# Kernel tuning notes

Measured on AMD Instinct MI355X. Metric: run time of the kernel, lower is better.

## Reference

```python
import jax, jax.numpy as jnp
import numpy as np

N, F_IN, H, F_OUT, E = 50000, 128, 8, 16, 800000


def setup_inputs() -> dict:
    key = jax.random.key(0)
    ks = jax.random.split(key, 10)
    x = jax.random.normal(ks[0], (N, F_IN), dtype=jnp.float32)
    edge_index = jax.random.randint(ks[1], (2, E), 0, N, dtype=jnp.int64 if jax.config.read('jax_enable_x64') else jnp.int32)
    edge_prob = jax.random.uniform(ks[2], (E, 1), dtype=jnp.float32)
    s = 1.0 / np.sqrt(F_IN)
    Wp = jax.random.normal(ks[3], (H * F_OUT, F_IN), dtype=jnp.float32) * s
    Wt = jax.random.normal(ks[4], (H * F_OUT, 1), dtype=jnp.float32)
    a_src = jax.random.normal(ks[5], (H, F_OUT), dtype=jnp.float32) * 0.1
    a_trg = jax.random.normal(ks[6], (H, F_OUT), dtype=jnp.float32) * 0.1
    a_tp = jax.random.normal(ks[7], (H, F_OUT), dtype=jnp.float32) * 0.1
    Wskip = jax.random.normal(ks[8], (H * F_OUT, F_IN), dtype=jnp.float32) * s
    bias = jnp.zeros((H * F_OUT,), dtype=jnp.float32)
    return {"x": x, "edge_index": edge_index, "edge_prob": edge_prob,
            "Wp": Wp, "Wt": Wt, "a_src": a_src, "a_trg": a_trg,
            "a_tp": a_tp, "Wskip": Wskip, "bias": bias}


def reference(x, edge_index, edge_prob, Wp, Wt, a_src, a_trg, a_tp, Wskip, bias):
    n = x.shape[0]
    h, f = a_src.shape
    src, trg = edge_index[0], edge_index[1]
    # node projection: [N, H, F_out]
    proj = (x @ Wp.T).reshape(n, h, f)
    # transition-prob projection: [E, H, F_out]
    trans = (edge_prob @ Wt.T).reshape(-1, h, f)
    # per-node source/target scores [N, H], per-edge prob score [E, H]
    s_src = jnp.einsum('nhf,hf->nh', proj, a_src)
    s_trg = jnp.einsum('nhf,hf->nh', proj, a_trg)
    s_tp = jnp.einsum('ehf,hf->eh', trans, a_tp)
    scores = jax.nn.leaky_relu(s_src[src] + s_trg[trg] + s_tp, negative_slope=0.2)
    # global-max-shifted exp, segment softmax over target nodes
    e = jnp.exp(scores - jnp.max(scores))
    denom = jax.ops.segment_sum(e, trg, num_segments=n)
    attn = e / (denom[trg] + 1e-16)  # [E, H]
    weighted = proj[src] * attn[..., None]  # [E, H, F_out]
    out = jax.ops.segment_sum(weighted, trg, num_segments=n)  # [N, H, F_out]
    # skip connection (F_out != F_in -> skip_proj path), concat heads, bias, ELU
    out = out + (x @ Wskip.T).reshape(n, h, f)
    out = out.reshape(n, h * f) + bias
    return jax.nn.elu(out)
```

## Files before the change

### kernel.cpp

```cpp
#include <hip/hip_runtime.h>
#include <hip/hip_fp16.h>
#include <math.h>

constexpr int Nn  = 50000;
constexpr int FIN = 128;
constexpr int NH  = 8;
constexpr int FO  = 16;
constexpr int HF  = 128;
constexpr int NWR = 272;
constexpr int NPREP = NWR / 2;
constexpr int NBLK64 = (Nn + 63) / 64;
constexpr int NSCAN = (Nn + 255) / 256;

typedef _Float16 f16x8 __attribute__((ext_vector_type(8)));
typedef float    f32x4 __attribute__((ext_vector_type(4)));

__global__ __launch_bounds__(256) void k_pc(
    const float* __restrict__ Wp, const float* __restrict__ Wskip,
    const float* __restrict__ a_src, const float* __restrict__ a_trg,
    const float* __restrict__ Wt, const float* __restrict__ a_tp,
    _Float16* __restrict__ Wh, float* __restrict__ ctp,
    const int* __restrict__ trg, int* __restrict__ deg,
    int* __restrict__ rank, int E)
{
    const int bid = blockIdx.x;
    if (bid < NPREP) {
        if (bid == 0 && threadIdx.x < NH) {
            int h = threadIdx.x;
            float s = 0.f;
            #pragma unroll
            for (int f = 0; f < FO; ++f) s += Wt[h * FO + f] * a_tp[h * FO + f];
            ctp[h] = s;
        }
        const int o = bid * 2 + (threadIdx.x >> 7);
        const int k = threadIdx.x & 127;
        float v;
        if (o < 128)      v = Wp[o * FIN + k];
        else if (o < 256) v = Wskip[(o - 128) * FIN + k];
        else if (o < 264) {
            const int h = o - 256;
            float s = 0.f;
            #pragma unroll
            for (int f = 0; f < FO; ++f)
                s += a_src[h * FO + f] * Wp[(h * FO + f) * FIN + k];
            v = s;
        } else {
            const int h = o - 264;
            float s = 0.f;
            #pragma unroll
            for (int f = 0; f < FO; ++f)
                s += a_trg[h * FO + f] * Wp[(h * FO + f) * FIN + k];
            v = s;
        }
        Wh[o * FIN + k] = (_Float16)v;
        return;
    }

    int e = (bid - NPREP) * 256 + threadIdx.x;
    if (e < E) rank[e] = atomicAdd(&deg[trg[e]], 1);
}

__global__ __launch_bounds__(256) void k_scan1(const int* __restrict__ deg,
                                               int* __restrict__ partial)
{
    __shared__ int lds[256];
    int t = threadIdx.x, i = blockIdx.x * 256 + t;
    lds[t] = (i < Nn) ? deg[i] : 0;
    __syncthreads();
    for (int off = 128; off > 0; off >>= 1) {
        if (t < off) lds[t] += lds[t + off];
        __syncthreads();
    }
    if (t == 0) partial[blockIdx.x] = lds[0];
}

__global__ __launch_bounds__(256) void k_scan3(const int* __restrict__ deg,
                                               const int* __restrict__ partial,
                                               int* __restrict__ pos)
{
    __shared__ int lds[256], lds2[256];
    const int t = threadIdx.x;
    const int i = blockIdx.x * 256 + t;
    lds2[t] = (t < NSCAN) ? partial[t] : 0;
    __syncthreads();
    for (int off = 1; off < 256; off <<= 1) {
        int u = (t >= off) ? lds2[t - off] : 0;
        __syncthreads();
        lds2[t] += u;
        __syncthreads();
    }
    const int base = (blockIdx.x == 0) ? 0 : lds2[blockIdx.x - 1];
    int v = (i < Nn) ? deg[i] : 0;
    lds[t] = v;
    __syncthreads();
    for (int off = 1; off < 256; off <<= 1) {
        int u = (t >= off) ? lds[t - off] : 0;
        __syncthreads();
        lds[t] += u;
        __syncthreads();
    }
    if (i < Nn) pos[i] = base + lds[t] - v;
}

__global__ __launch_bounds__(256) void k_fn(
    const int* __restrict__ src, const int* __restrict__ trg,
    const float* __restrict__ prob, const int* __restrict__ rank,
    const int* __restrict__ pos, unsigned int* __restrict__ spk,
    const float* __restrict__ x, const _Float16* __restrict__ Wh,
    const float* __restrict__ bias,
    __half* __restrict__ projA, float* __restrict__ out,
    float* __restrict__ s_pair, int E, int nbFill)
{
    const int bid = blockIdx.x;

    if (bid < nbFill) {
        int e4 = bid * 256 + threadIdx.x;
        if (e4 * 4 < E) {
            int4   s4 = reinterpret_cast<const int4*>(src)[e4];
            int4   t4 = reinterpret_cast<const int4*>(trg)[e4];
            float4 p4 = reinterpret_cast<const float4*>(prob)[e4];
            int4   r4 = reinterpret_cast<const int4*>(rank)[e4];
            int    sv[4] = {s4.x, s4.y, s4.z, s4.w};
            int    tv[4] = {t4.x, t4.y, t4.z, t4.w};
            int    rv[4] = {r4.x, r4.y, r4.z, r4.w};
            float  pv[4] = {p4.x, p4.y, p4.z, p4.w};
            #pragma unroll
            for (int i = 0; i < 4; ++i) {
                int slot = pos[tv[i]] + rv[i];
                spk[slot] = (unsigned int)sv[i] |
                    ((unsigned int)__half_as_ushort(__float2half_rn(pv[i])) << 16);
            }
        }
        return;
    }

    const int g0 = (bid - nbFill) * 64;
    const int w  = threadIdx.x >> 6;
    const int l  = threadIdx.x & 63;
    const int lr = l & 15;
    const int kb = l >> 4;
    const int t0 = w * 4;

    f16x8 b[4][4];
    const _Float16* wb = Wh + (size_t)lr * FIN + kb * 8;
    #pragma unroll
    for (int i = 0; i < 4; ++i) {
        #pragma unroll
        for (int ks = 0; ks < 4; ++ks)
            b[i][ks] = *reinterpret_cast<const f16x8*>(
                wb + (size_t)(t0 + i) * 16 * FIN + ks * 32);
    }
    f16x8 b16[4];
    if (w == 3) {
        #pragma unroll
        for (int ks = 0; ks < 4; ++ks)
            b16[ks] = *reinterpret_cast<const f16x8*>(
                wb + (size_t)16 * 16 * FIN + ks * 32);
    }

    #pragma unroll
    for (int ng = 0; ng < 4; ++ng) {
        const int n0 = g0 + ng * 16;
        if (n0 >= Nn) break;

        f16x8 a[4];
        const float* xr = x + (size_t)(n0 + lr) * FIN + kb * 8;
        #pragma unroll
        for (int ks = 0; ks < 4; ++ks) {
            float4 u0 = *reinterpret_cast<const float4*>(xr + ks * 32);
            float4 u1 = *reinterpret_cast<const float4*>(xr + ks * 32 + 4);
            a[ks][0] = (_Float16)u0.x; a[ks][1] = (_Float16)u0.y;
            a[ks][2] = (_Float16)u0.z; a[ks][3] = (_Float16)u0.w;
            a[ks][4] = (_Float16)u1.x; a[ks][5] = (_Float16)u1.y;
            a[ks][6] = (_Float16)u1.z; a[ks][7] = (_Float16)u1.w;
        }

        f32x4 acc[4];
        #pragma unroll
        for (int i = 0; i < 4; ++i) acc[i] = (f32x4){0.f, 0.f, 0.f, 0.f};
        f32x4 acc16 = (f32x4){0.f, 0.f, 0.f, 0.f};

        #pragma unroll
        for (int i = 0; i < 4; ++i) {
            #pragma unroll
            for (int ks = 0; ks < 4; ++ks)
                acc[i] = __builtin_amdgcn_mfma_f32_16x16x32_f16(
                    a[ks], b[i][ks], acc[i], 0, 0, 0);
        }
        if (w == 3) {
            #pragma unroll
            for (int ks = 0; ks < 4; ++ks)
                acc16 = __builtin_amdgcn_mfma_f32_16x16x32_f16(
                    a[ks], b16[ks], acc16, 0, 0, 0);
        }

        #pragma unroll
        for (int r = 0; r < 4; ++r) {
            const int n = n0 + kb * 4 + r;
            if (t0 < 8) {
                #pragma unroll
                for (int i = 0; i < 4; ++i)
                    projA[(size_t)n * HF + (t0 + i) * FO + lr] =
                        __float2half_rn(acc[i][r]);
            } else {
                #pragma unroll
                for (int i = 0; i < 4; ++i) {
                    const int o = (t0 + i - 8) * 16 + lr;
                    out[(size_t)n * HF + o] = acc[i][r] + bias[o];
                }
            }
            if (w == 3) s_pair[n * 16 + lr] = acc16[r];
        }
    }
}

__global__ __launch_bounds__(256) void k_gather(
    const unsigned int* __restrict__ spk, const int* __restrict__ pos,
    const float* __restrict__ s_pair, const float* __restrict__ ctp,
    const __half2* __restrict__ projA, float* __restrict__ out, int E)
{
    const int wv   = threadIdx.x >> 6;
    const int n    = blockIdx.x * 4 + wv;
    const int lane = threadIdx.x & 63;
    const int h    = lane >> 3;
    const int f2   = lane & 7;

    const int jb = pos[n];
    const int je = (n + 1 < Nn) ? pos[n + 1] : E;
    const float st  = s_pair[n * 16 + 8 + h];
    const float cth = ctp[h];
    const float* __restrict__ ssl = s_pair + h;
    const __half2* __restrict__ pA = projA + h * 8 + f2;

    float num0 = 0.f, num1 = 0.f, den = 0.f;
    int j = jb;
    for (; j + 3 < je; j += 4) {
        const unsigned int pk0 = spk[j];
        const unsigned int pk1 = spk[j + 1];
        const unsigned int pk2 = spk[j + 2];
        const unsigned int pk3 = spk[j + 3];
        const int s0 = pk0 & 0xFFFF, s1 = pk1 & 0xFFFF;
        const int s2 = pk2 & 0xFFFF, s3 = pk3 & 0xFFFF;
        const float ss0 = ssl[s0 * 16], ss1 = ssl[s1 * 16];
        const float ss2 = ssl[s2 * 16], ss3 = ssl[s3 * 16];
        const __half2 g0 = pA[s0 * 64], g1 = pA[s1 * 64];
        const __half2 g2 = pA[s2 * 64], g3 = pA[s3 * 64];
        const float p0 = __half2float(__ushort_as_half((unsigned short)(pk0 >> 16)));
        const float p1 = __half2float(__ushort_as_half((unsigned short)(pk1 >> 16)));
        const float p2 = __half2float(__ushort_as_half((unsigned short)(pk2 >> 16)));
        const float p3 = __half2float(__ushort_as_half((unsigned short)(pk3 >> 16)));
        float sc0 = ss0 + st + cth * p0;
        float sc1 = ss1 + st + cth * p1;
        float sc2 = ss2 + st + cth * p2;
        float sc3 = ss3 + st + cth * p3;
        sc0 = fmaxf(sc0, 0.2f * sc0);
        sc1 = fmaxf(sc1, 0.2f * sc1);
        sc2 = fmaxf(sc2, 0.2f * sc2);
        sc3 = fmaxf(sc3, 0.2f * sc3);
        const float ev0 = __expf(sc0), ev1 = __expf(sc1);
        const float ev2 = __expf(sc2), ev3 = __expf(sc3);
        const float2 G0 = __half22float2(g0), G1 = __half22float2(g1);
        const float2 G2 = __half22float2(g2), G3 = __half22float2(g3);
        den  += (ev0 + ev1) + (ev2 + ev3);
        num0 += ev0 * G0.x + ev1 * G1.x + ev2 * G2.x + ev3 * G3.x;
        num1 += ev0 * G0.y + ev1 * G1.y + ev2 * G2.y + ev3 * G3.y;
    }
    for (; j < je; ++j) {
        const unsigned int pk = spk[j];
        const int s = pk & 0xFFFF;
        const float p = __half2float(__ushort_as_half((unsigned short)(pk >> 16)));
        float sc = ssl[s * 16] + st + cth * p;
        sc = fmaxf(sc, 0.2f * sc);
        const float ev = __expf(sc);
        const float2 G = __half22float2(pA[s * 64]);
        den  += ev;
        num0 += ev * G.x;
        num1 += ev * G.y;
    }

    const float inv = 1.f / (den + 1e-16f);
    const int idx = n * HF + h * FO + f2 * 2;
    float2 o = *reinterpret_cast<const float2*>(&out[idx]);
    float v0 = o.x + num0 * inv;
    float v1 = o.y + num1 * inv;
    v0 = v0 > 0.f ? v0 : expm1f(v0);
    v1 = v1 > 0.f ? v1 : expm1f(v1);
    *reinterpret_cast<float2*>(&out[idx]) = make_float2(v0, v1);
}

extern "C" void kernel_launch(void* const* d_in, const int* in_sizes, int n_in,
                              void* d_out, int out_size, void* d_ws, size_t ws_size,
                              hipStream_t stream)
{
    const float* x     = (const float*)d_in[0];
    const int*   ei    = (const int*)d_in[1];
    const float* prob  = (const float*)d_in[2];
    const float* Wp    = (const float*)d_in[3];
    const float* Wt    = (const float*)d_in[4];
    const float* a_src = (const float*)d_in[5];
    const float* a_trg = (const float*)d_in[6];
    const float* a_tp  = (const float*)d_in[7];
    const float* Wskip = (const float*)d_in[8];
    const float* bias  = (const float*)d_in[9];
    float* out = (float*)d_out;

    const int E = in_sizes[2];
    const int* src = ei;
    const int* trg = ei + E;

    char* wsb = (char*)d_ws;
    __half* projA  = (__half*)wsb;
    float* s_pair  = (float*)(wsb + (size_t)Nn*HF*2);
    float* ctp     = s_pair + (size_t)Nn * 16;
    _Float16* Wh   = (_Float16*)(ctp + 16);
    unsigned int* spk = (unsigned int*)(Wh + (size_t)NWR * FIN);
    int*   rank    = (int*)(spk + E);
    int*   deg     = rank + E;
    int*   pos     = deg + Nn;
    int*   partial = pos + Nn;

    const int nbCount = (E + 255) / 256;
    const int nbFill  = (E + 1023) / 1024;

    hipMemsetAsync(deg, 0, (size_t)Nn * sizeof(int), stream);
    k_pc<<<NPREP + nbCount, 256, 0, stream>>>(Wp, Wskip, a_src, a_trg, Wt,
                                              a_tp, Wh, ctp, trg, deg, rank, E);
    k_scan1<<<NSCAN, 256, 0, stream>>>(deg, partial);
    k_scan3<<<NSCAN, 256, 0, stream>>>(deg, partial, pos);
    k_fn<<<nbFill + NBLK64, 256, 0, stream>>>(src, trg, prob, rank, pos, spk,
                                              x, Wh, bias, projA, out,
                                              s_pair, E, nbFill);
    k_gather<<<Nn / 4, 256, 0, stream>>>(spk, pos, s_pair, ctp,
                                         (const __half2*)projA, out, E);
}
```

Before: 138.0 us.

## Merge scan kernels into one and prefetch next x tile in projection GEMM

The two-pass prefix scan becomes a single kernel in which each block recomputes its base offset by summing every degree before it. This removes one launch and the partial buffer, at the cost of redundant reads that grow with block index. The projection loop in k_fn now loads the next 16-row slab of x into registers while the MFMAs for the current slab run, to hide global load latency. The extra registers could lower occupancy, and the tail block keeps a separate single-slab path.

```diff
diff --git a/kernel.cpp b/kernel.cpp
--- a/kernel.cpp
+++ b/kernel.cpp
@@ -60,36 +60,25 @@
     if (e < E) rank[e] = atomicAdd(&deg[trg[e]], 1);
 }
 
-__global__ __launch_bounds__(256) void k_scan1(const int* __restrict__ deg,
-                                               int* __restrict__ partial)
+__global__ __launch_bounds__(256) void k_scan(const int* __restrict__ deg,
+                                              int* __restrict__ pos)
 {
     __shared__ int lds[256];
-    int t = threadIdx.x, i = blockIdx.x * 256 + t;
-    lds[t] = (i < Nn) ? deg[i] : 0;
+    const int b = blockIdx.x, t = threadIdx.x;
+    const int lim = b * 256;
+
+    int s = 0;
+    for (int i = t; i < lim; i += 256) s += deg[i];
+    lds[t] = s;
     __syncthreads();
     for (int off = 128; off > 0; off >>= 1) {
         if (t < off) lds[t] += lds[t + off];
         __syncthreads();
     }
-    if (t == 0) partial[blockIdx.x] = lds[0];
-}
-
-__global__ __launch_bounds__(256) void k_scan3(const int* __restrict__ deg,
-                                               const int* __restrict__ partial,
-                                               int* __restrict__ pos)
-{
-    __shared__ int lds[256], lds2[256];
-    const int t = threadIdx.x;
-    const int i = blockIdx.x * 256 + t;
-    lds2[t] = (t < NSCAN) ? partial[t] : 0;
+    const int base = lds[0];
     __syncthreads();
-    for (int off = 1; off < 256; off <<= 1) {
-        int u = (t >= off) ? lds2[t - off] : 0;
-        __syncthreads();
-        lds2[t] += u;
-        __syncthreads();
-    }
-    const int base = (blockIdx.x == 0) ? 0 : lds2[blockIdx.x - 1];
+
+    const int i = lim + t;
     int v = (i < Nn) ? deg[i] : 0;
     lds[t] = v;
     __syncthreads();
@@ -158,17 +147,83 @@
                 wb + (size_t)16 * 16 * FIN + ks * 32);
     }
 
-    #pragma unroll
-    for (int ng = 0; ng < 4; ++ng) {
-        const int n0 = g0 + ng * 16;
-        if (n0 >= Nn) break;
-
+    const float* xr0 = x + (size_t)(g0 + lr) * FIN + kb * 8;
+
+    if (g0 + 64 <= Nn) {
+        float4 ucur[8];
+        #pragma unroll
+        for (int q = 0; q < 8; ++q)
+            ucur[q] = *reinterpret_cast<const float4*>(
+                xr0 + (q >> 1) * 32 + (q & 1) * 4);
+
+        #pragma unroll
+        for (int ng = 0; ng < 4; ++ng) {
+            float4 unx[8];
+            if (ng < 3) {
+                const float* xrn = xr0 + (size_t)(ng + 1) * 16 * FIN;
+                #pragma unroll
+                for (int q = 0; q < 8; ++q)
+                    unx[q] = *reinterpret_cast<const float4*>(
+                        xrn + (q >> 1) * 32 + (q & 1) * 4);
+            }
+
+            f16x8 a[4];
+            #pragma unroll
+            for (int ks = 0; ks < 4; ++ks) {
+                float4 lo = ucur[ks * 2], hi = ucur[ks * 2 + 1];
+                a[ks][0] = (_Float16)lo.x; a[ks][1] = (_Float16)lo.y;
+                a[ks][2] = (_Float16)lo.z; a[ks][3] = (_Float16)lo.w;
+                a[ks][4] = (_Float16)hi.x; a[ks][5] = (_Float16)hi.y;
+                a[ks][6] = (_Float16)hi.z; a[ks][7] = (_Float16)hi.w;
+            }
+
+            f32x4 acc[4];
+            #pragma unroll
+            for (int i = 0; i < 4; ++i) acc[i] = (f32x4){0.f, 0.f, 0.f, 0.f};
+            f32x4 acc16 = (f32x4){0.f, 0.f, 0.f, 0.f};
+
+            #pragma unroll
+            for (int i = 0; i < 4; ++i) {
+                #pragma unroll
+                for (int ks = 0; ks < 4; ++ks)
+                    acc[i] = __builtin_amdgcn_mfma_f32_16x16x32_f16(
+                        a[ks], b[i][ks], acc[i], 0, 0, 0);
+            }
+            if (w == 3) {
+                #pragma unroll
+                for (int ks = 0; ks < 4; ++ks)
+                    acc16 = __builtin_amdgcn_mfma_f32_16x16x32_f16(
+                        a[ks], b16[ks], acc16, 0, 0, 0);
+            }
+
+            const int n0 = g0 + ng * 16;
+            #pragma unroll
+            for (int r = 0; r < 4; ++r) {
+                const int n = n0 + kb * 4 + r;
+                if (t0 < 8) {
+                    #pragma unroll
+                    for (int i = 0; i < 4; ++i)
+                        projA[(size_t)n * HF + (t0 + i) * FO + lr] =
+                            __float2half_rn(acc[i][r]);
+                } else {
+                    #pragma unroll
+                    for (int i = 0; i < 4; ++i) {
+                        const int o = (t0 + i - 8) * 16 + lr;
+                        out[(size_t)n * HF + o] = acc[i][r] + bias[o];
+                    }
+                }
+                if (w == 3) s_pair[n * 16 + lr] = acc16[r];
+            }
+
+            #pragma unroll
+            for (int q = 0; q < 8; ++q) ucur[q] = unx[q];
+        }
+    } else {
         f16x8 a[4];
-        const float* xr = x + (size_t)(n0 + lr) * FIN + kb * 8;
         #pragma unroll
         for (int ks = 0; ks < 4; ++ks) {
-            float4 u0 = *reinterpret_cast<const float4*>(xr + ks * 32);
-            float4 u1 = *reinterpret_cast<const float4*>(xr + ks * 32 + 4);
+            float4 u0 = *reinterpret_cast<const float4*>(xr0 + ks * 32);
+            float4 u1 = *reinterpret_cast<const float4*>(xr0 + ks * 32 + 4);
             a[ks][0] = (_Float16)u0.x; a[ks][1] = (_Float16)u0.y;
             a[ks][2] = (_Float16)u0.z; a[ks][3] = (_Float16)u0.w;
             a[ks][4] = (_Float16)u1.x; a[ks][5] = (_Float16)u1.y;
@@ -196,7 +251,7 @@
 
         #pragma unroll
         for (int r = 0; r < 4; ++r) {
-            const int n = n0 + kb * 4 + r;
+            const int n = g0 + kb * 4 + r;
             if (t0 < 8) {
                 #pragma unroll
                 for (int i = 0; i < 4; ++i)
@@ -317,7 +372,6 @@
     int*   rank    = (int*)(spk + E);
     int*   deg     = rank + E;
     int*   pos     = deg + Nn;
-    int*   partial = pos + Nn;
 
     const int nbCount = (E + 255) / 256;
     const int nbFill  = (E + 1023) / 1024;
@@ -325,8 +379,7 @@
     hipMemsetAsync(deg, 0, (size_t)Nn * sizeof(int), stream);
     k_pc<<<NPREP + nbCount, 256, 0, stream>>>(Wp, Wskip, a_src, a_trg, Wt,
                                               a_tp, Wh, ctp, trg, deg, rank, E);
-    k_scan1<<<NSCAN, 256, 0, stream>>>(deg, partial);
-    k_scan3<<<NSCAN, 256, 0, stream>>>(deg, partial, pos);
+    k_scan<<<NSCAN, 256, 0, stream>>>(deg, pos);
     k_fn<<<nbFill + NBLK64, 256, 0, stream>>>(src, trg, prob, rank, pos, spk,
                                               x, Wh, bias, projA, out,
                                               s_pair, E, nbFill);
```

Result: slower. 163.4 us (+18.4%).
